# Kernel tuning notes

Measured on AMD Instinct MI355X. Metric: run time of the kernel, lower is better.

Reference implementation:

```python
import jax, jax.numpy as jnp
import numpy as np


def setup_inputs() -> dict:
    key = jax.random.key(0)
    kq, kk, kv = jax.random.split(key, 3)
    n, m, d, v = 4096, 4096, 1024, 1024
    Q = jax.random.normal(kq, (n, d), dtype=jnp.float32)
    K = jax.random.normal(kk, (m, d), dtype=jnp.float32)
    V = jax.random.normal(kv, (m, v), dtype=jnp.float32)
    return {"Q": Q, "K": K, "V": V}


def reference(Q, K, V):
    d = K.shape[-1]
    scale = d ** (-0.5)
    logits = jnp.matmul(Q, K.T)                      # [n, m]
    # Faithful to source: softmax over dim=1 (keys), THEN scaled by d**-0.5
    scores = jax.nn.softmax(logits, axis=1) * scale  # [n, m]
    return jnp.matmul(scores, V)                     # [n, v]
```

## Files before the change

kernel.cpp:

```cpp
#include <hip/hip_runtime.h>
#include <hip/hip_bf16.h>

typedef _Float16 f16x8 __attribute__((ext_vector_type(8)));
typedef _Float16 f16x4 __attribute__((ext_vector_type(4)));
typedef float f32x4 __attribute__((ext_vector_type(4)));

__device__ __forceinline__ void async_ld16(_Float16* lds, const _Float16* g) {
    __builtin_amdgcn_global_load_lds(
        (const __attribute__((address_space(1))) void*)g,
        (__attribute__((address_space(3))) void*)lds, 16, 0, 0);
}

#define VMCNT(n) asm volatile("s_waitcnt vmcnt(" #n ")" ::: "memory")
#define LGKMCNT0 asm volatile("s_waitcnt lgkmcnt(0)" ::: "memory")
#define BAR() __builtin_amdgcn_s_barrier()

__global__ __launch_bounds__(512, 2) void gemm_bt256(
    const _Float16* __restrict__ A,
    const _Float16* __restrict__ B,
    float* __restrict__ C,
    int M, int N, int K, int Ks)
{
    __shared__ _Float16 Asm[2][256 * 64];
    __shared__ _Float16 Bsm[2][256 * 64];

    const int tid  = threadIdx.x;
    const int w    = tid >> 6;
    const int lane = tid & 63;
    const int l16  = lane & 15;
    const int quad = lane >> 4;
    const int wm   = w >> 2;
    const int wn   = w & 3;

    const int gx = gridDim.x, gy = gridDim.y;
    const int total = gx * gy * (int)gridDim.z;
    int lid = (int)blockIdx.x + gx * ((int)blockIdx.y + gy * (int)blockIdx.z);
    {
        const int q = total >> 3, r = total & 7;
        const int xcd = lid & 7, i = lid >> 3;
        lid = (xcd < r ? xcd * (q + 1) : r * (q + 1) + (xcd - r) * q) + i;
    }
    const int bx = lid % gx;
    const int by = (lid / gx) % gy;
    const int bz = lid / (gx * gy);

    const int row0 = by * 256;
    const int col0 = bx * 256;

    const _Float16* Ab = A + (size_t)row0 * K + (size_t)bz * Ks;
    const _Float16* Bb = B + (size_t)col0 * K + (size_t)bz * Ks;

    const int lr = lane >> 3;
    const int lc = (lane & 7) ^ lr;
    const size_t soff  = (size_t)(w * 16 + lr) * K + lc * 8;
    const _Float16* pa = Ab + soff;
    const _Float16* pb = Bb + soff;
    const size_t jstep = (size_t)8 * K;
    const size_t hstep = (size_t)128 * K;

    auto STAGE = [&](_Float16* sm, const _Float16* gsrc, int h, int kcol) {
        _Float16* d = sm + h * 8192 + w * 1024;
        const _Float16* s = gsrc + (size_t)h * hstep + kcol;
        async_ld16(d,       s);
        async_ld16(d + 512, s + jstep);
    };

    const int abase = (wm * 16 + l16) * 64;
    const int bbase = (wn * 16 + l16) * 64;
    const int rs0   = ((quad)     ^ (l16 & 7)) * 8;
    const int rs1   = ((4 + quad) ^ (l16 & 7)) * 8;

#define READ_A(dst, msoff)                                                     \
    _Pragma("unroll")                                                          \
    for (int m_ = 0; m_ < 4; ++m_) {                                           \
        dst[m_][0] = *(const f16x8*)(abuf + (msoff) + m_ * 2048 + abase + rs0);\
        dst[m_][1] = *(const f16x8*)(abuf + (msoff) + m_ * 2048 + abase + rs1);\
    }
#define READ_B(dst, nsoff)                                                     \
    _Pragma("unroll")                                                          \
    for (int n_ = 0; n_ < 2; ++n_) {                                           \
        dst[n_][0] = *(const f16x8*)(bbuf + (nsoff) + n_ * 4096 + bbase + rs0);\
        dst[n_][1] = *(const f16x8*)(bbuf + (nsoff) + n_ * 4096 + bbase + rs1);\
    }
#define MFMA4x2(accrow, afrag, bfrag, bcol)                                    \
    _Pragma("unroll")                                                          \
    for (int m_ = 0; m_ < 4; ++m_)                                             \
      _Pragma("unroll")                                                        \
      for (int n_ = 0; n_ < 2; ++n_) {                                         \
        acc[(accrow) + m_][(bcol) + n_] =                                      \
            __builtin_amdgcn_mfma_f32_16x16x32_f16(                            \
                afrag[m_][0], bfrag[n_][0], acc[(accrow) + m_][(bcol) + n_],   \
                0, 0, 0);                                                      \
        acc[(accrow) + m_][(bcol) + n_] =                                      \
            __builtin_amdgcn_mfma_f32_16x16x32_f16(                            \
                afrag[m_][1], bfrag[n_][1], acc[(accrow) + m_][(bcol) + n_],   \
                0, 0, 0);                                                      \
      }

    f32x4 acc[8][4] = {};
    const int NT = Ks >> 6;

    STAGE(&Asm[0][0], pa, 0, 0);
    STAGE(&Bsm[0][0], pb, 0, 0);
    STAGE(&Bsm[0][0], pb, 1, 0);
    STAGE(&Asm[0][0], pa, 1, 0);
    if (NT > 1) {
        STAGE(&Asm[1][0], pa, 0, 64);
        STAGE(&Bsm[1][0], pb, 0, 64);
        STAGE(&Bsm[1][0], pb, 1, 64);
        VMCNT(6);
    } else {
        VMCNT(0);
    }
    BAR();

    for (int t = 0; t < NT; ++t) {
        const int buf = t & 1;
        const _Float16* abuf = &Asm[buf][0];
        const _Float16* bbuf = &Bsm[buf][0];
        _Float16* const acur = &Asm[buf][0];
        _Float16* const bcur = &Bsm[buf][0];
        _Float16* const anxt = &Asm[buf ^ 1][0];

        f16x8 alo[4][2], ahi[4][2], blo[2][2], bhi[2][2];

        READ_A(alo, 0);
        READ_B(blo, 0);
        if (t + 1 < NT) STAGE(anxt, pa, 1, (t + 1) * 64);
        BAR();
        LGKMCNT0;
        __builtin_amdgcn_s_setprio(1);
        MFMA4x2(0, alo, blo, 0);
        __builtin_amdgcn_s_setprio(0);
        BAR();

        READ_B(bhi, 8192);
        if (t + 2 < NT) STAGE(acur, pa, 0, (t + 2) * 64);
        BAR();
        LGKMCNT0;
        __builtin_amdgcn_s_setprio(1);
        MFMA4x2(0, alo, bhi, 2);
        __builtin_amdgcn_s_setprio(0);
        BAR();

        READ_A(ahi, 8192);
        if (t + 2 < NT) STAGE(bcur, pb, 0, (t + 2) * 64);
        BAR();
        LGKMCNT0;
        __builtin_amdgcn_s_setprio(1);
        MFMA4x2(4, ahi, bhi, 2);
        __builtin_amdgcn_s_setprio(0);
        BAR();

        if (t + 2 < NT) STAGE(bcur, pb, 1, (t + 2) * 64);
        BAR();
        __builtin_amdgcn_s_setprio(1);
        MFMA4x2(4, ahi, blo, 0);
        __builtin_amdgcn_s_setprio(0);
        if (t + 2 < NT) { VMCNT(6); } else { VMCNT(0); }
        BAR();
    }

    float* Cb = C + (size_t)bz * ((size_t)M * N);
    #pragma unroll
    for (int i = 0; i < 8; ++i) {
        const int ms = i >> 2, m = i & 3;
        const int gr = row0 + ms * 128 + m * 32 + wm * 16 + quad * 4;
        #pragma unroll
        for (int j = 0; j < 4; ++j) {
            const int ns = j >> 1, nn = j & 1;
            const int gc = col0 + ns * 128 + nn * 64 + wn * 16 + l16;
            const f32x4 v = acc[i][j];
            #pragma unroll
            for (int e = 0; e < 4; ++e)
                Cb[(size_t)(gr + e) * N + gc] = v[e];
        }
    }
#undef READ_A
#undef READ_B
#undef MFMA4x2
}

__global__ __launch_bounds__(256) void gemm_bt(
    const _Float16* __restrict__ A,
    const _Float16* __restrict__ B,
    float* __restrict__ C,
    int M, int N, int K, int Ks)
{
    __shared__ _Float16 At[2][128 * 32];
    __shared__ _Float16 Bt[2][128 * 32];

    const int tid  = threadIdx.x;
    const int wave = tid >> 6;
    const int lane = tid & 63;

    int gx = gridDim.x, gy = gridDim.y;
    int bx = blockIdx.x, by = blockIdx.y;
    if (((gx & 7) == 0) && ((gy & 7) == 0)) {
        const int bid    = bx + gx * by;
        const int ntx    = gx >> 3;
        const int sid    = bid >> 6;
        const int within = bid & 63;
        const int sx = sid % ntx;
        const int sy = sid / ntx;
        bx = (sx << 3) + (within & 7);
        by = (sy << 3) + (within >> 3);
    }
    const int row0 = by * 128;
    const int col0 = bx * 128;

    const int wr = (wave >> 1) * 64;
    const int wc = (wave & 1) * 64;
    const int quad = lane >> 4;
    const int l16  = lane & 15;

    f32x4 acc[4][4] = {};

    const int srow  = lane >> 2;
    const int skoff = (lane & 3) * 8;
    const size_t K64 = (size_t)64 * K;

    const _Float16* Ab = A + (size_t)row0 * K + (size_t)blockIdx.z * Ks;
    const _Float16* Bb = B + (size_t)col0 * K + (size_t)blockIdx.z * Ks;
    float* Cb = C + (size_t)blockIdx.z * M * N;

    const _Float16* pa = Ab + (size_t)(wave * 16 + srow) * K + skoff;
    const _Float16* pb = Bb + (size_t)(wave * 16 + srow) * K + skoff;

    async_ld16(At[0] + wave * 512,       pa);
    async_ld16(At[0] + (wave + 4) * 512, pa + K64);
    async_ld16(Bt[0] + wave * 512,       pb);
    async_ld16(Bt[0] + (wave + 4) * 512, pb + K64);
    __syncthreads();

    int cur = 0;
    for (int k0 = 0; k0 < Ks; k0 += 32) {
        const int nxt = cur ^ 1;
        if (k0 + 32 < Ks) {
            const _Float16* qa = pa + k0 + 32;
            const _Float16* qb = pb + k0 + 32;
            async_ld16(At[nxt] + wave * 512,       qa);
            async_ld16(At[nxt] + (wave + 4) * 512, qa + K64);
            async_ld16(Bt[nxt] + wave * 512,       qb);
            async_ld16(Bt[nxt] + (wave + 4) * 512, qb + K64);
        }

        f16x8 af[4], bf[4];
        #pragma unroll
        for (int r = 0; r < 4; ++r)
            af[r] = *(const f16x8*)&At[cur][(wr + r * 16 + l16) * 32 + quad * 8];
        #pragma unroll
        for (int c = 0; c < 4; ++c)
            bf[c] = *(const f16x8*)&Bt[cur][(wc + c * 16 + l16) * 32 + quad * 8];

        #pragma unroll
        for (int r = 0; r < 4; ++r)
            #pragma unroll
            for (int c = 0; c < 4; ++c)
                acc[r][c] = __builtin_amdgcn_mfma_f32_16x16x32_f16(af[r], bf[c], acc[r][c], 0, 0, 0);

        __syncthreads();
        cur = nxt;
    }

    #pragma unroll
    for (int r = 0; r < 4; ++r) {
        const int growb = row0 + wr + r * 16 + quad * 4;
        #pragma unroll
        for (int c = 0; c < 4; ++c) {
            const int gcol = col0 + wc + c * 16 + l16;
            #pragma unroll
            for (int i = 0; i < 4; ++i)
                Cb[(size_t)(growb + i) * N + gcol] = acc[r][c][i];
        }
    }
}

__global__ __launch_bounds__(256) void softmax_rows(
    const float* __restrict__ S, _Float16* __restrict__ P, float scale)
{
    __shared__ float red[4];
    const int row = blockIdx.x;
    const int tid = threadIdx.x;
    const int wave = tid >> 6;
    const float4* Sr = (const float4*)(S + (size_t)row * 4096);

    float4 x[4];
    #pragma unroll
    for (int i = 0; i < 4; ++i) x[i] = Sr[tid + i * 256];

    float mx = -3.402823466e+38f;
    #pragma unroll
    for (int i = 0; i < 4; ++i)
        mx = fmaxf(mx, fmaxf(fmaxf(x[i].x, x[i].y), fmaxf(x[i].z, x[i].w)));
    #pragma unroll
    for (int off = 32; off > 0; off >>= 1) mx = fmaxf(mx, __shfl_down(mx, off));
    if ((tid & 63) == 0) red[wave] = mx;
    __syncthreads();
    mx = fmaxf(fmaxf(red[0], red[1]), fmaxf(red[2], red[3]));
    __syncthreads();

    float sum = 0.0f;
    #pragma unroll
    for (int i = 0; i < 4; ++i) {
        x[i].x = __expf(x[i].x - mx);
        x[i].y = __expf(x[i].y - mx);
        x[i].z = __expf(x[i].z - mx);
        x[i].w = __expf(x[i].w - mx);
        sum += x[i].x + x[i].y + x[i].z + x[i].w;
    }
    #pragma unroll
    for (int off = 32; off > 0; off >>= 1) sum += __shfl_down(sum, off);
    if ((tid & 63) == 0) red[wave] = sum;
    __syncthreads();
    sum = red[0] + red[1] + red[2] + red[3];

    const float inv = scale / sum;
    f16x4* Pr = (f16x4*)(P + (size_t)row * 4096);
    #pragma unroll
    for (int i = 0; i < 4; ++i) {
        f16x4 h;
        h.x = (_Float16)(x[i].x * inv);
        h.y = (_Float16)(x[i].y * inv);
        h.z = (_Float16)(x[i].z * inv);
        h.w = (_Float16)(x[i].w * inv);
        Pr[tid + i * 256] = h;
    }
}

__global__ __launch_bounds__(256) void cvt2_f32_f16(
    const float4* __restrict__ a, f16x4* __restrict__ da, int n4a,
    const float4* __restrict__ b, f16x4* __restrict__ db, int n4b)
{
    int i = blockIdx.x * 256 + threadIdx.x;
    const int stride = gridDim.x * 256;
    const int tot = n4a + n4b;
    for (; i < tot; i += stride) {
        const float4* s = (i < n4a) ? (a + i) : (b + (i - n4a));
        f16x4* d = (i < n4a) ? (da + i) : (db + (i - n4a));
        float4 v = *s;
        f16x4 h;
        h.x = (_Float16)v.x; h.y = (_Float16)v.y;
        h.z = (_Float16)v.z; h.w = (_Float16)v.w;
        *d = h;
    }
}

__global__ __launch_bounds__(256) void transpose_cvt(
    const float* __restrict__ V, _Float16* __restrict__ Vt, int rows, int cols)
{
    __shared__ float tile[32][33];
    const int c0 = blockIdx.x * 32;
    const int r0 = blockIdx.y * 32;
    const int tx = threadIdx.x & 31;
    const int ty = threadIdx.x >> 5;
    #pragma unroll
    for (int i = 0; i < 4; ++i)
        tile[ty * 4 + i][tx] = V[(size_t)(r0 + ty * 4 + i) * cols + c0 + tx];
    __syncthreads();
    #pragma unroll
    for (int i = 0; i < 4; ++i)
        Vt[(size_t)(c0 + ty * 4 + i) * rows + r0 + tx] = (_Float16)tile[tx][ty * 4 + i];
}

__global__ __launch_bounds__(256) void reduce2(
    const float4* __restrict__ a, const float4* __restrict__ b,
    float4* __restrict__ o, int n4)
{
    int i = blockIdx.x * 256 + threadIdx.x;
    const int stride = gridDim.x * 256;
    for (; i < n4; i += stride) {
        float4 u = a[i], v = b[i];
        float4 w;
        w.x = u.x + v.x; w.y = u.y + v.y; w.z = u.z + v.z; w.w = u.w + v.w;
        o[i] = w;
    }
}

__global__ __launch_bounds__(256) void reduce4(
    const float4* __restrict__ a, const float4* __restrict__ b,
    const float4* __restrict__ c, const float4* __restrict__ d,
    float4* __restrict__ o, int n4)
{
    int i = blockIdx.x * 256 + threadIdx.x;
    const int stride = gridDim.x * 256;
    for (; i < n4; i += stride) {
        float4 u = a[i], v = b[i], x = c[i], y = d[i];
        float4 w;
        w.x = (u.x + v.x) + (x.x + y.x);
        w.y = (u.y + v.y) + (x.y + y.y);
        w.z = (u.z + v.z) + (x.z + y.z);
        w.w = (u.w + v.w) + (x.w + y.w);
        o[i] = w;
    }
}

extern "C" void kernel_launch(void* const* d_in, const int* in_sizes, int n_in,
                              void* d_out, int out_size, void* d_ws, size_t ws_size,
                              hipStream_t stream) {
    const float* Q = (const float*)d_in[0];
    const float* K = (const float*)d_in[1];
    const float* V = (const float*)d_in[2];
    float* out = (float*)d_out;

    const int n = 4096, m = 4096, d = 1024, vdim = 1024;
    const float scale = 0.03125f;

    char* w = (char*)d_ws;
    _Float16* Qh = (_Float16*)w;
    _Float16* Kh = (_Float16*)(w + (8u << 20));
    _Float16* Vt = (_Float16*)(w + (16u << 20));
    char* rest = w + (24u << 20);
    size_t avail = ws_size > (24u << 20) ? ws_size - (24u << 20) : 0;

    int nc = 128;
    if      ((size_t)4096 * m * 6 <= avail) nc = 4096;
    else if ((size_t)2048 * m * 6 <= avail) nc = 2048;
    else if ((size_t)1024 * m * 6 <= avail) nc = 1024;
    else if ((size_t)512  * m * 6 <= avail) nc = 512;
    else if ((size_t)256  * m * 6 <= avail) nc = 256;

    float*    S = (float*)rest;
    _Float16* P = (_Float16*)(rest + (size_t)nc * m * 4);
    float* part = S;

    cvt2_f32_f16<<<dim3(2048), dim3(256), 0, stream>>>(
        (const float4*)Q, (f16x4*)Qh, n * d / 4,
        (const float4*)K, (f16x4*)Kh, m * d / 4);
    transpose_cvt<<<dim3(vdim / 32, m / 32), dim3(256), 0, stream>>>(V, Vt, m, vdim);

    if (nc >= 256) {
        for (int r0 = 0; r0 < n; r0 += nc) {
            gemm_bt256<<<dim3(m / 256, nc / 256, 1), dim3(512), 0, stream>>>(
                Qh + (size_t)r0 * d, Kh, S, nc, m, d, d);
            softmax_rows<<<dim3(nc), dim3(256), 0, stream>>>(S, P, scale);
            gemm_bt256<<<dim3(vdim / 256, nc / 256, 4), dim3(512), 0, stream>>>(
                P, Vt, part, nc, vdim, m, m / 4);
            reduce4<<<dim3(1024), dim3(256), 0, stream>>>(
                (const float4*)part,
                (const float4*)(part + (size_t)nc * vdim),
                (const float4*)(part + (size_t)2 * nc * vdim),
                (const float4*)(part + (size_t)3 * nc * vdim),
                (float4*)(out + (size_t)r0 * vdim), nc * vdim / 4);
        }
    } else {
        for (int r0 = 0; r0 < n; r0 += nc) {
            gemm_bt<<<dim3(m / 128, nc / 128, 1), dim3(256), 0, stream>>>(
                Qh + (size_t)r0 * d, Kh, S, nc, m, d, d);
            softmax_rows<<<dim3(nc), dim3(256), 0, stream>>>(S, P, scale);
            gemm_bt<<<dim3(vdim / 128, nc / 128, 2), dim3(256), 0, stream>>>(
                P, Vt, part, nc, vdim, m, m / 2);
            reduce2<<<dim3(1024), dim3(256), 0, stream>>>(
                (const float4*)part, (const float4*)(part + (size_t)nc * vdim),
                (float4*)(out + (size_t)r0 * vdim), nc * vdim / 4);
        }
    }
}
```

Measured before the change: 199.0 us.

## Software-pipeline LDS fragment reads across GEMM k-iterations and drop explicit lgkmcnt waits

Moves the first A/B fragment reads of the next k-tile to the end of the current iteration, after the vmcnt wait. It also issues the bhi/ahi LDS reads one phase earlier so they overlap with the preceding MFMA block. The explicit lgkmcnt(0) waits are removed, leaving LDS wait insertion to the compiler. This aims to hide LDS read latency behind MFMA work. The cost is more live fragment registers. There is also a risk that the next-buffer reads happen before the barrier that guarantees other waves' async global-to-LDS loads have landed.

```diff
diff --git a/kernel.cpp b/kernel.cpp
--- a/kernel.cpp
+++ b/kernel.cpp
@@ -12,7 +12,6 @@
 }
 
 #define VMCNT(n) asm volatile("s_waitcnt vmcnt(" #n ")" ::: "memory")
-#define LGKMCNT0 asm volatile("s_waitcnt lgkmcnt(0)" ::: "memory")
 #define BAR() __builtin_amdgcn_s_barrier()
 
 __global__ __launch_bounds__(512, 2) void gemm_bt256(
@@ -70,17 +69,17 @@
     const int rs0   = ((quad)     ^ (l16 & 7)) * 8;
     const int rs1   = ((4 + quad) ^ (l16 & 7)) * 8;
 
-#define READ_A(dst, msoff)                                                     \
+#define READ_A(dst, bufp, msoff)                                               \
     _Pragma("unroll")                                                          \
     for (int m_ = 0; m_ < 4; ++m_) {                                           \
-        dst[m_][0] = *(const f16x8*)(abuf + (msoff) + m_ * 2048 + abase + rs0);\
-        dst[m_][1] = *(const f16x8*)(abuf + (msoff) + m_ * 2048 + abase + rs1);\
-    }
-#define READ_B(dst, nsoff)                                                     \
+        dst[m_][0] = *(const f16x8*)((bufp) + (msoff) + m_ * 2048 + abase + rs0);\
+        dst[m_][1] = *(const f16x8*)((bufp) + (msoff) + m_ * 2048 + abase + rs1);\
+    }
+#define READ_B(dst, bufp, nsoff)                                               \
     _Pragma("unroll")                                                          \
     for (int n_ = 0; n_ < 2; ++n_) {                                           \
-        dst[n_][0] = *(const f16x8*)(bbuf + (nsoff) + n_ * 4096 + bbase + rs0);\
-        dst[n_][1] = *(const f16x8*)(bbuf + (nsoff) + n_ * 4096 + bbase + rs1);\
+        dst[n_][0] = *(const f16x8*)((bufp) + (nsoff) + n_ * 4096 + bbase + rs0);\
+        dst[n_][1] = *(const f16x8*)((bufp) + (nsoff) + n_ * 4096 + bbase + rs1);\
     }
 #define MFMA4x2(accrow, afrag, bfrag, bcol)                                    \
     _Pragma("unroll")                                                          \
@@ -114,6 +113,10 @@
     }
     BAR();
 
+    f16x8 alo[4][2], ahi[4][2], blo[2][2], bhi[2][2];
+    READ_A(alo, &Asm[0][0], 0);
+    READ_B(blo, &Bsm[0][0], 0);
+
     for (int t = 0; t < NT; ++t) {
         const int buf = t & 1;
         const _Float16* abuf = &Asm[buf][0];
@@ -122,31 +125,24 @@
         _Float16* const bcur = &Bsm[buf][0];
         _Float16* const anxt = &Asm[buf ^ 1][0];
 
-        f16x8 alo[4][2], ahi[4][2], blo[2][2], bhi[2][2];
-
-        READ_A(alo, 0);
-        READ_B(blo, 0);
+        READ_B(bhi, bbuf, 8192);
         if (t + 1 < NT) STAGE(anxt, pa, 1, (t + 1) * 64);
         BAR();
-        LGKMCNT0;
         __builtin_amdgcn_s_setprio(1);
         MFMA4x2(0, alo, blo, 0);
         __builtin_amdgcn_s_setprio(0);
         BAR();
 
-        READ_B(bhi, 8192);
+        READ_A(ahi, abuf, 8192);
         if (t + 2 < NT) STAGE(acur, pa, 0, (t + 2) * 64);
         BAR();
-        LGKMCNT0;
         __builtin_amdgcn_s_setprio(1);
         MFMA4x2(0, alo, bhi, 2);
         __builtin_amdgcn_s_setprio(0);
         BAR();
 
-        READ_A(ahi, 8192);
         if (t + 2 < NT) STAGE(bcur, pb, 0, (t + 2) * 64);
         BAR();
-        LGKMCNT0;
         __builtin_amdgcn_s_setprio(1);
         MFMA4x2(4, ahi, bhi, 2);
         __builtin_amdgcn_s_setprio(0);
@@ -158,6 +154,12 @@
         MFMA4x2(4, ahi, blo, 0);
         __builtin_amdgcn_s_setprio(0);
         if (t + 2 < NT) { VMCNT(6); } else { VMCNT(0); }
+        if (t + 1 < NT) {
+            const _Float16* nab = &Asm[buf ^ 1][0];
+            const _Float16* nbb = &Bsm[buf ^ 1][0];
+            READ_A(alo, nab, 0);
+            READ_B(blo, nbb, 0);
+        }
         BAR();
     }
 
```

Result: slower. 203.9 us (+2.5%).
